# Performance work log

Measured on AMD Instinct MI355X. Metric: run time of the kernel, lower is better.

The kernel has to match this reference:

```python
import jax, jax.numpy as jnp
import numpy as np

N = 50000      # nodes
E = 800000     # edges (before self-loops)
B = 512        # graphs in batch
IN, HID, OUT, HEADS = 768, 256, 128, 4
NEG_SLOPE = 0.2
EPS = 1e-16


def glorot(key, shape):
    fan = shape[0] + shape[-1]
    return jax.random.normal(key, shape, jnp.float32) * jnp.sqrt(2.0 / fan)


def setup_inputs() -> dict:
    key = jax.random.key(0)
    ks = jax.random.split(key, 12)
    d1, d2 = HID // HEADS, OUT // HEADS
    return {
        "x": jax.random.normal(ks[0], (N, IN), jnp.float32),
        "edge_index": jax.random.randint(ks[1], (2, E), 0, N),
        "batch": jnp.sort(jax.random.randint(ks[2], (N,), 0, B)),
        # conv1: GATConv(IN, HID//HEADS, heads=HEADS)
        "W1": glorot(ks[3], (IN, HID)),
        "att_src1": glorot(ks[4], (HEADS, d1)),
        "att_dst1": glorot(ks[5], (HEADS, d1)),
        "b1": jnp.zeros((HID,), jnp.float32),
        # conv2: GATConv(HID+IN, OUT//HEADS, heads=HEADS)
        "W2": glorot(ks[6], (HID + IN, OUT)),
        "att_src2": glorot(ks[7], (HEADS, d2)),
        "att_dst2": glorot(ks[8], (HEADS, d2)),
        "b2": jnp.zeros((OUT,), jnp.float32),
    }


def gat_conv(x, src, dst, W, att_src, att_dst, bias):
    # PyG GATConv (concat heads): h = x @ W, e_ij = LeakyReLU(a_s.h_j + a_d.h_i),
    # alpha = softmax over incoming edges of each destination node.
    n = x.shape[0]
    heads, d = att_src.shape
    h = (x @ W).reshape(n, heads, d)                          # [N,H,D]
    a_s = jnp.einsum('nhd,hd->nh', h, att_src)                # [N,H]
    a_d = jnp.einsum('nhd,hd->nh', h, att_dst)
    e = jax.nn.leaky_relu(a_s[src] + a_d[dst], NEG_SLOPE)     # [Etot,H]
    e_max = jax.ops.segment_max(e, dst, num_segments=n)
    e = jnp.exp(e - e_max[dst])
    denom = jax.ops.segment_sum(e, dst, num_segments=n)
    alpha = e / (denom[dst] + EPS)                            # [Etot,H]
    msg = h[src] * alpha[:, :, None]                          # [Etot,H,D]
    out = jax.ops.segment_sum(msg, dst, num_segments=n)       # [N,H,D]
    return out.reshape(n, heads * d) + bias


def reference(x, edge_index, batch, W1, att_src1, att_dst1, b1,
              W2, att_src2, att_dst2, b2):
    # BUrumorGAT swaps edge direction: row<->col
    src = edge_index[1]
    dst = edge_index[0]
    # PyG GATConv adds self-loops by default
    loops = jnp.arange(N)
    src = jnp.concatenate([src, loops])
    dst = jnp.concatenate([dst, loops])

    x1 = x  # original features
    h1 = gat_conv(x, src, dst, W1, att_src1, att_dst1, b1)    # [N,HID]
    x2 = h1

    # root of each graph = first node (in order) with that batch id
    roots = jax.ops.segment_min(jnp.arange(N), batch, num_segments=B)  # [B]
    re1 = x1[roots[batch]]                                    # [N,IN]
    xc = jax.nn.relu(jnp.concatenate([h1, re1], axis=1))      # [N,HID+IN]
    # F.dropout with training=False is identity (eval mode)

    h2 = jax.nn.relu(gat_conv(xc, src, dst, W2, att_src2, att_dst2, b2))  # [N,OUT]
    re2 = x2[roots[batch]]                                    # [N,HID]
    feat = jnp.concatenate([h2, re2], axis=1)                 # [N,OUT+HID]

    counts = jax.ops.segment_sum(jnp.ones((N,), jnp.float32), batch, num_segments=B)
    pooled = jax.ops.segment_sum(feat, batch, num_segments=B)
    return pooled / jnp.clip(counts, 1.0)[:, None]            # [B,OUT+HID]
```

## Files before the change

kernel.cpp:

```cpp
#include <hip/hip_runtime.h>

#define NN 50000
#define NBGRAPH 512
#define DIN 768
#define DHID 256
#define DOUT 128

typedef unsigned short ushort_t;
typedef __attribute__((ext_vector_type(4))) float f32x4;
typedef _Float16 f16_t;
typedef __attribute__((ext_vector_type(8))) _Float16 f16x8;

__device__ __forceinline__ float lrelu(float v) { return v > 0.f ? v : 0.2f * v; }

__device__ __forceinline__ float h2f_u(ushort_t u) { return (float)__builtin_bit_cast(f16_t, u); }
__device__ __forceinline__ ushort_t f2h_u(float f) { return __builtin_bit_cast(ushort_t, (f16_t)f); }

__device__ __forceinline__ float sel_h(int h, float q0, float q1, float q2, float q3) {
  float lo = (h & 1) ? q1 : q0;
  float hi = (h & 1) ? q3 : q2;
  return (h & 2) ? hi : lo;
}

__device__ __forceinline__ f16x8 cvt8(float4 u, float4 v) {
  unsigned int a = __builtin_bit_cast(unsigned int, __builtin_amdgcn_cvt_pkrtz(u.x, u.y));
  unsigned int b = __builtin_bit_cast(unsigned int, __builtin_amdgcn_cvt_pkrtz(u.z, u.w));
  unsigned int c = __builtin_bit_cast(unsigned int, __builtin_amdgcn_cvt_pkrtz(v.x, v.y));
  unsigned int d = __builtin_bit_cast(unsigned int, __builtin_amdgcn_cvt_pkrtz(v.z, v.w));
  uint4 q = {a, b, c, d};
  return __builtin_bit_cast(f16x8, q);
}
__device__ __forceinline__ f16x8 cvt8_relu(float4 u, float4 v) {
  u.x = fmaxf(u.x, 0.f); u.y = fmaxf(u.y, 0.f); u.z = fmaxf(u.z, 0.f); u.w = fmaxf(u.w, 0.f);
  v.x = fmaxf(v.x, 0.f); v.y = fmaxf(v.y, 0.f); v.z = fmaxf(v.z, 0.f); v.w = fmaxf(v.w, 0.f);
  return cvt8(u, v);
}

__device__ __forceinline__ void gl_lds16(const void* g, void* l) {
  __builtin_amdgcn_global_load_lds(
      (const __attribute__((address_space(1))) unsigned int*)g,
      (__attribute__((address_space(3))) unsigned int*)l, 16, 0, 0);
}

__global__ void k_zero2(int* __restrict__ a, int* __restrict__ b, int n) {
  int i = blockIdx.x * blockDim.x + threadIdx.x;
  if (i < n) { a[i] = 0; b[i] = 0; }
}

__global__ void k_hist(const int* __restrict__ ei, int* __restrict__ deg, int E, int Etot) {
  int e = blockIdx.x * blockDim.x + threadIdx.x;
  if (e >= Etot) return;
  int dst = (e < E) ? ei[e] : (e - E);
  atomicAdd(&deg[dst], 1);
}

__global__ __launch_bounds__(1024) void k_scan1(const int* __restrict__ deg, int* __restrict__ off,
                                                int* __restrict__ bsum, int n) {
  __shared__ int wsum[16];
  int tid = threadIdx.x, lane = tid & 63, w = tid >> 6;
  int i = blockIdx.x * 1024 + tid;
  int v = (i < n) ? deg[i] : 0;
  int x = v;
#pragma unroll
  for (int d = 1; d < 64; d <<= 1) { int t = __shfl_up(x, d); if (lane >= d) x += t; }
  if (lane == 63) wsum[w] = x;
  __syncthreads();
  if (tid < 16) {
    int y = wsum[tid];
#pragma unroll
    for (int d = 1; d < 16; d <<= 1) { int t = __shfl_up(y, d); if (tid >= d) y += t; }
    wsum[tid] = y;
  }
  __syncthreads();
  int base = (w > 0) ? wsum[w - 1] : 0;
  if (i < n) off[i] = base + x - v;
  if (tid == 1023) bsum[blockIdx.x] = wsum[15];
}

__global__ void k_scan2(int* __restrict__ bsum, int* __restrict__ off, int nb, int n) {
  int lane = threadIdx.x;
  int v = (lane < nb) ? bsum[lane] : 0;
  int x = v;
#pragma unroll
  for (int d = 1; d < 64; d <<= 1) { int t = __shfl_up(x, d); if (lane >= d) x += t; }
  if (lane < nb) bsum[lane] = x - v;
  if (lane == 63) off[n] = x;
}

__global__ void k_scan3(int* __restrict__ off, const int* __restrict__ bsum, int n) {
  int i = blockIdx.x * blockDim.x + threadIdx.x;
  if (i < n) off[i] += bsum[i >> 10];
}

__global__ void k_scatter(const int* __restrict__ ei, const int* __restrict__ off,
                          int* __restrict__ cur, int* __restrict__ csr, int E, int Etot) {
  int e = blockIdx.x * blockDim.x + threadIdx.x;
  if (e >= Etot) return;
  int dst, src;
  if (e < E) { dst = ei[e]; src = ei[E + e]; }
  else       { dst = src = e - E; }
  int p = atomicAdd(&cur[dst], 1);
  csr[off[dst] + p] = src;
}

__global__ void k_segstart(const int* __restrict__ batch, int* __restrict__ segstart, int n, int b_cnt) {
  int b = blockIdx.x * blockDim.x + threadIdx.x;
  if (b > b_cnt) return;
  int lo = 0, hi = n;
  while (lo < hi) { int mid = (lo + hi) >> 1; if (batch[mid] < b) lo = mid + 1; else hi = mid; }
  segstart[b] = lo;
}

__global__ void k_rootn(const int* __restrict__ batch, const int* __restrict__ segstart,
                        int* __restrict__ rootn, int n) {
  int i = blockIdx.x * blockDim.x + threadIdx.x;
  if (i < n) rootn[i] = segstart[batch[i]];
}

__global__ void k_prepW(const float* __restrict__ W, ushort_t* __restrict__ Wt, int K, int N) {
  int id = blockIdx.x * blockDim.x + threadIdx.x;
  if (id >= K * N) return;
  int n = id / K, k = id - n * K;
  Wt[(size_t)n * K + k] = f2h_u(W[(size_t)k * N + n]);
}

#define ABUF1 (128 * 32)
#define BBUF1 (128 * 32)
__global__ __launch_bounds__(256) void k_gemm1m(const float* __restrict__ A,
                                                const ushort_t* __restrict__ Bt,
                                                ushort_t* __restrict__ C) {
  const int K = DIN, NC = DHID;
  __shared__ __align__(16) float As[2 * ABUF1];
  __shared__ __align__(16) ushort_t Bs[2 * BBUF1];
  const int tid = threadIdx.x;
  const int bm = blockIdx.x * 128;
  const int bn = blockIdx.y * 128;
  const int wid = tid >> 6, lane = tid & 63;
  const int wr = (wid >> 1) * 64, wc = (wid & 1) * 64;
  const int fr = lane & 15, fg = lane >> 4;
  f32x4 acc[4][4] = {};

  const float* asrc[4];
  int adoff[4];
#pragma unroll
  for (int j = 0; j < 4; ++j) {
    int c = j * 256 + tid;
    int row = c >> 3, ci = c & 7;
    int gc = ci ^ (row & 7);
    int gr = bm + row; if (gr >= NN) gr = NN - 1;
    asrc[j] = &A[(size_t)gr * K + gc * 4];
    adoff[j] = row * 32 + ci * 4;
  }
  const ushort_t* bsrc[2];
  int bdoff[2];
#pragma unroll
  for (int j = 0; j < 2; ++j) {
    int c = j * 256 + tid;
    int col = c >> 2, ci = c & 3;
    int gc = ci ^ (col & 3);
    bsrc[j] = &Bt[(size_t)(bn + col) * K + gc * 8];
    bdoff[j] = col * 32 + ci * 8;
  }

#pragma unroll
  for (int j = 0; j < 4; ++j) gl_lds16(asrc[j], &As[adoff[j]]);
#pragma unroll
  for (int j = 0; j < 2; ++j) gl_lds16(bsrc[j], &Bs[bdoff[j]]);
  __syncthreads();

  int cur = 0;
  for (int k0 = 0; k0 < K; k0 += 32) {
    const int nxt = cur ^ 1;
    if (k0 + 32 < K) {
#pragma unroll
      for (int j = 0; j < 4; ++j) gl_lds16(asrc[j] + k0 + 32, &As[nxt * ABUF1 + adoff[j]]);
#pragma unroll
      for (int j = 0; j < 2; ++j) gl_lds16(bsrc[j] + k0 + 32, &Bs[nxt * BBUF1 + bdoff[j]]);
    }
    const float* Ab = &As[cur * ABUF1];
    const ushort_t* Bb = &Bs[cur * BBUF1];
    f16x8 af[4], bfr[4];
#pragma unroll
    for (int m = 0; m < 4; ++m) {
      int r = wr + m * 16 + fr;
      int c0 = (2 * fg) ^ (r & 7), c1 = (2 * fg + 1) ^ (r & 7);
      float4 u = *(const float4*)&Ab[r * 32 + c0 * 4];
      float4 v = *(const float4*)&Ab[r * 32 + c1 * 4];
      af[m] = cvt8(u, v);
    }
#pragma unroll
    for (int n = 0; n < 4; ++n) {
      int c = wc + n * 16 + fr;
      bfr[n] = *(const f16x8*)&Bb[c * 32 + (fg ^ (c & 3)) * 8];
    }
#pragma unroll
    for (int m = 0; m < 4; ++m)
#pragma unroll
      for (int n = 0; n < 4; ++n)
        acc[m][n] = __builtin_amdgcn_mfma_f32_16x16x32_f16(af[m], bfr[n], acc[m][n], 0, 0, 0);
    __syncthreads();
    cur = nxt;
  }
#pragma unroll
  for (int m = 0; m < 4; ++m)
#pragma unroll
    for (int n = 0; n < 4; ++n)
#pragma unroll
      for (int j = 0; j < 4; ++j) {
        int r = bm + wr + m * 16 + fg * 4 + j;
        if (r < NN) C[(size_t)r * NC + bn + wc + n * 16 + fr] = f2h_u(acc[m][n][j]);
      }
}

#define ABUF2 (64 * 32)
#define BBUF2 (128 * 32)
__global__ __launch_bounds__(256) void k_gemm2m(const float* __restrict__ OUT1,
                                                const float* __restrict__ X,
                                                const int* __restrict__ rootn,
                                                const ushort_t* __restrict__ Bt,
                                                ushort_t* __restrict__ C) {
  const int K = DHID + DIN, NC = DOUT;
  __shared__ __align__(16) float As[2 * ABUF2];
  __shared__ __align__(16) ushort_t Bs[2 * BBUF2];
  const int tid = threadIdx.x;
  const int bm = blockIdx.x * 64;
  const int wid = tid >> 6, lane = tid & 63;
  const int wr = (wid >> 1) * 32, wc = (wid & 1) * 64;
  const int fr = lane & 15, fg = lane >> 4;
  f32x4 acc[2][4] = {};

  const float* o1src[2];
  const float* xsrc[2];
  int adoff[2];
#pragma unroll
  for (int j = 0; j < 2; ++j) {
    int c = j * 256 + tid;
    int row = c >> 3, ci = c & 7;
    int gc = ci ^ (row & 7);
    int gr = bm + row; if (gr >= NN) gr = NN - 1;
    int rn = rootn[gr];
    o1src[j] = &OUT1[(size_t)gr * DHID + gc * 4];
    xsrc[j] = &X[(size_t)rn * DIN + gc * 4];
    adoff[j] = row * 32 + ci * 4;
  }
  const ushort_t* bsrc[2];
  int bdoff[2];
#pragma unroll
  for (int j = 0; j < 2; ++j) {
    int c = j * 256 + tid;
    int col = c >> 2, ci = c & 3;
    int gc = ci ^ (col & 3);
    bsrc[j] = &Bt[(size_t)col * K + gc * 8];
    bdoff[j] = col * 32 + ci * 8;
  }

#pragma unroll
  for (int j = 0; j < 2; ++j) gl_lds16(o1src[j], &As[adoff[j]]);
#pragma unroll
  for (int j = 0; j < 2; ++j) gl_lds16(bsrc[j], &Bs[bdoff[j]]);
  __syncthreads();

  int cur = 0;
  for (int k0 = 0; k0 < K; k0 += 32) {
    const int nxt = cur ^ 1;
    if (k0 + 32 < K) {
      const int k0n = k0 + 32;
      const bool inO1 = k0n < DHID;
#pragma unroll
      for (int j = 0; j < 2; ++j)
        gl_lds16(inO1 ? (o1src[j] + k0n) : (xsrc[j] + (k0n - DHID)), &As[nxt * ABUF2 + adoff[j]]);
#pragma unroll
      for (int j = 0; j < 2; ++j) gl_lds16(bsrc[j] + k0n, &Bs[nxt * BBUF2 + bdoff[j]]);
    }
    const float* Ab = &As[cur * ABUF2];
    const ushort_t* Bb = &Bs[cur * BBUF2];
    f16x8 af[2], bfr[4];
#pragma unroll
    for (int m = 0; m < 2; ++m) {
      int r = wr + m * 16 + fr;
      int c0 = (2 * fg) ^ (r & 7), c1 = (2 * fg + 1) ^ (r & 7);
      float4 u = *(const float4*)&Ab[r * 32 + c0 * 4];
      float4 v = *(const float4*)&Ab[r * 32 + c1 * 4];
      af[m] = cvt8_relu(u, v);
    }
#pragma unroll
    for (int n = 0; n < 4; ++n) {
      int c = wc + n * 16 + fr;
      bfr[n] = *(const f16x8*)&Bb[c * 32 + (fg ^ (c & 3)) * 8];
    }
#pragma unroll
    for (int m = 0; m < 2; ++m)
#pragma unroll
      for (int n = 0; n < 4; ++n)
        acc[m][n] = __builtin_amdgcn_mfma_f32_16x16x32_f16(af[m], bfr[n], acc[m][n], 0, 0, 0);
    __syncthreads();
    cur = nxt;
  }
#pragma unroll
  for (int m = 0; m < 2; ++m)
#pragma unroll
    for (int n = 0; n < 4; ++n)
#pragma unroll
      for (int j = 0; j < 4; ++j) {
        int r = bm + wr + m * 16 + fg * 4 + j;
        if (r < NN) C[(size_t)r * NC + wc + n * 16 + fr] = f2h_u(acc[m][n][j]);
      }
}

__global__ __launch_bounds__(256) void k_scores1(const ushort_t* __restrict__ Hh,
                                                 const float* __restrict__ att_s,
                                                 const float* __restrict__ att_d,
                                                 float4* __restrict__ as_out,
                                                 float4* __restrict__ ad_out) {
  int lane = threadIdx.x & 63;
  int n = blockIdx.x * 4 + (threadIdx.x >> 6);
  if (n >= NN) return;
  ushort4 hv = *(const ushort4*)&Hh[(size_t)n * DHID + lane * 4];
  float h0 = h2f_u(hv.x), h1 = h2f_u(hv.y), h2 = h2f_u(hv.z), h3 = h2f_u(hv.w);
  float4 sa = *(const float4*)&att_s[lane * 4];
  float4 da = *(const float4*)&att_d[lane * 4];
  float ps = h0 * sa.x + h1 * sa.y + h2 * sa.z + h3 * sa.w;
  float pd = h0 * da.x + h1 * da.y + h2 * da.z + h3 * da.w;
#pragma unroll
  for (int m = 1; m < 16; m <<= 1) { ps += __shfl_xor(ps, m); pd += __shfl_xor(pd, m); }
  float4 rs, rd;
  rs.x = __shfl(ps, 0);  rd.x = __shfl(pd, 0);
  rs.y = __shfl(ps, 16); rd.y = __shfl(pd, 16);
  rs.z = __shfl(ps, 32); rd.z = __shfl(pd, 32);
  rs.w = __shfl(ps, 48); rd.w = __shfl(pd, 48);
  if (lane == 0) { as_out[n] = rs; ad_out[n] = rd; }
}

__global__ __launch_bounds__(256) void k_scores2(const ushort_t* __restrict__ Hh,
                                                 const float* __restrict__ att_s,
                                                 const float* __restrict__ att_d,
                                                 float4* __restrict__ as_out,
                                                 float4* __restrict__ ad_out) {
  int lane = threadIdx.x & 63;
  int n = blockIdx.x * 4 + (threadIdx.x >> 6);
  if (n >= NN) return;
  ushort2 hv = *(const ushort2*)&Hh[(size_t)n * DOUT + lane * 2];
  float h0 = h2f_u(hv.x), h1 = h2f_u(hv.y);
  float2 sa = *(const float2*)&att_s[lane * 2];
  float2 da = *(const float2*)&att_d[lane * 2];
  float ps = h0 * sa.x + h1 * sa.y;
  float pd = h0 * da.x + h1 * da.y;
#pragma unroll
  for (int m = 1; m < 16; m <<= 1) { ps += __shfl_xor(ps, m); pd += __shfl_xor(pd, m); }
  float4 rs, rd;
  rs.x = __shfl(ps, 0);  rd.x = __shfl(pd, 0);
  rs.y = __shfl(ps, 16); rd.y = __shfl(pd, 16);
  rs.z = __shfl(ps, 32); rd.z = __shfl(pd, 32);
  rs.w = __shfl(ps, 48); rd.w = __shfl(pd, 48);
  if (lane == 0) { as_out[n] = rs; ad_out[n] = rd; }
}

__global__ __launch_bounds__(256) void k_agg1(const int* __restrict__ off, const int* __restrict__ csr,
                                              const float4* __restrict__ as_v, const float4* __restrict__ ad_v,
                                              const ushort_t* __restrict__ Hh, const float* __restrict__ bias,
                                              float* __restrict__ OUT) {
  __shared__ int s_tab[16][65];
  __shared__ __align__(16) float al_tab[16][260];
  const int tid = threadIdx.x;
  const int nd = tid >> 4;
  const int g = tid & 15;
  const int hd = g >> 2;
  const int n = blockIdx.x * 16 + nd;
  if (n >= NN) return;
  const int beg = off[n];
  const int nt = off[n + 1] - beg;
  const float4 adv = ad_v[n];

  float acc[16] = {};
  float rdh;

  if (nt <= 64) {
    float mx0 = -INFINITY, mx1 = -INFINITY, mx2 = -INFINITY, mx3 = -INFINITY;
    for (int le = g; le < nt; le += 16) {
      int s = csr[beg + le];
      float4 a = as_v[s];
      s_tab[nd][le] = s;
      *(float4*)&al_tab[nd][le << 2] = a;
      mx0 = fmaxf(mx0, a.x); mx1 = fmaxf(mx1, a.y);
      mx2 = fmaxf(mx2, a.z); mx3 = fmaxf(mx3, a.w);
    }
#pragma unroll
    for (int m = 1; m < 16; m <<= 1) {
      mx0 = fmaxf(mx0, __shfl_xor(mx0, m)); mx1 = fmaxf(mx1, __shfl_xor(mx1, m));
      mx2 = fmaxf(mx2, __shfl_xor(mx2, m)); mx3 = fmaxf(mx3, __shfl_xor(mx3, m));
    }
    float em0 = lrelu(mx0 + adv.x), em1 = lrelu(mx1 + adv.y);
    float em2 = lrelu(mx2 + adv.z), em3 = lrelu(mx3 + adv.w);
    float s0 = 0.f, s1 = 0.f, s2 = 0.f, s3 = 0.f;
    for (int le = g; le < nt; le += 16) {
      float4 a = *(const float4*)&al_tab[nd][le << 2];
      float p0 = __expf(lrelu(a.x + adv.x) - em0);
      float p1 = __expf(lrelu(a.y + adv.y) - em1);
      float p2 = __expf(lrelu(a.z + adv.z) - em2);
      float p3 = __expf(lrelu(a.w + adv.w) - em3);
      *(float4*)&al_tab[nd][le << 2] = make_float4(p0, p1, p2, p3);
      s0 += p0; s1 += p1; s2 += p2; s3 += p3;
    }
#pragma unroll
    for (int m = 1; m < 16; m <<= 1) {
      s0 += __shfl_xor(s0, m); s1 += __shfl_xor(s1, m);
      s2 += __shfl_xor(s2, m); s3 += __shfl_xor(s3, m);
    }
    rdh = sel_h(hd, 1.f / (s0 + 1e-16f), 1.f / (s1 + 1e-16f),
                    1.f / (s2 + 1e-16f), 1.f / (s3 + 1e-16f));

    int sP = s_tab[nd][0];
    float pP = al_tab[nd][hd];
    f16x8 v0 = *(const f16x8*)&Hh[(size_t)sP * DHID + g * 16];
    f16x8 v1 = *(const f16x8*)&Hh[(size_t)sP * DHID + g * 16 + 8];
    for (int e = 0; e < nt; ++e) {
      int en = (e + 1 < nt) ? e + 1 : e;
      int sN = s_tab[nd][en];
      float pN = al_tab[nd][(en << 2) | hd];
      f16x8 n0 = *(const f16x8*)&Hh[(size_t)sN * DHID + g * 16];
      f16x8 n1 = *(const f16x8*)&Hh[(size_t)sN * DHID + g * 16 + 8];
      float al = pP * rdh;
#pragma unroll
      for (int q = 0; q < 8; ++q) acc[q] += al * (float)v0[q];
#pragma unroll
      for (int q = 0; q < 8; ++q) acc[8 + q] += al * (float)v1[q];
      pP = pN; v0 = n0; v1 = n1;
    }
  } else {
    float mx0 = -INFINITY, mx1 = -INFINITY, mx2 = -INFINITY, mx3 = -INFINITY;
    for (int le = g; le < nt; le += 16) {
      float4 a = as_v[csr[beg + le]];
      mx0 = fmaxf(mx0, a.x); mx1 = fmaxf(mx1, a.y);
      mx2 = fmaxf(mx2, a.z); mx3 = fmaxf(mx3, a.w);
    }
#pragma unroll
    for (int m = 1; m < 16; m <<= 1) {
      mx0 = fmaxf(mx0, __shfl_xor(mx0, m)); mx1 = fmaxf(mx1, __shfl_xor(mx1, m));
      mx2 = fmaxf(mx2, __shfl_xor(mx2, m)); mx3 = fmaxf(mx3, __shfl_xor(mx3, m));
    }
    float em0 = lrelu(mx0 + adv.x), em1 = lrelu(mx1 + adv.y);
    float em2 = lrelu(mx2 + adv.z), em3 = lrelu(mx3 + adv.w);
    float s0 = 0.f, s1 = 0.f, s2 = 0.f, s3 = 0.f;
    for (int le = g; le < nt; le += 16) {
      float4 a = as_v[csr[beg + le]];
      s0 += __expf(lrelu(a.x + adv.x) - em0);
      s1 += __expf(lrelu(a.y + adv.y) - em1);
      s2 += __expf(lrelu(a.z + adv.z) - em2);
      s3 += __expf(lrelu(a.w + adv.w) - em3);
    }
#pragma unroll
    for (int m = 1; m < 16; m <<= 1) {
      s0 += __shfl_xor(s0, m); s1 += __shfl_xor(s1, m);
      s2 += __shfl_xor(s2, m); s3 += __shfl_xor(s3, m);
    }
    rdh = sel_h(hd, 1.f / (s0 + 1e-16f), 1.f / (s1 + 1e-16f),
                    1.f / (s2 + 1e-16f), 1.f / (s3 + 1e-16f));
    float adh = sel_h(hd, adv.x, adv.y, adv.z, adv.w);
    float emh = sel_h(hd, em0, em1, em2, em3);
    for (int e = 0; e < nt; ++e) {
      int s = csr[beg + e];
      float4 a = as_v[s];
      float ah = sel_h(hd, a.x, a.y, a.z, a.w);
      float al = __expf(lrelu(ah + adh) - emh) * rdh;
      f16x8 v0 = *(const f16x8*)&Hh[(size_t)s * DHID + g * 16];
      f16x8 v1 = *(const f16x8*)&Hh[(size_t)s * DHID + g * 16 + 8];
#pragma unroll
      for (int q = 0; q < 8; ++q) acc[q] += al * (float)v0[q];
#pragma unroll
      for (int q = 0; q < 8; ++q) acc[8 + q] += al * (float)v1[q];
    }
  }

  const float* bv = &bias[g * 16];
  float* ob = &OUT[(size_t)n * DHID + g * 16];
#pragma unroll
  for (int k = 0; k < 4; ++k) {
    float4 b4 = *(const float4*)&bv[k * 4];
    *(float4*)&ob[k * 4] = make_float4(acc[k * 4] + b4.x, acc[k * 4 + 1] + b4.y,
                                       acc[k * 4 + 2] + b4.z, acc[k * 4 + 3] + b4.w);
  }
}

__global__ __launch_bounds__(256) void k_agg2(const int* __restrict__ off, const int* __restrict__ csr,
                                              const float4* __restrict__ as_v, const float4* __restrict__ ad_v,
                                              const ushort_t* __restrict__ Hh, const float* __restrict__ bias,
                                              float* __restrict__ OUT) {
  __shared__ int s_tab[16][65];
  __shared__ __align__(16) float al_tab[16][260];
  const int tid = threadIdx.x;
  const int nd = tid >> 4;
  const int g = tid & 15;
  const int hd = g >> 2;
  const int n = blockIdx.x * 16 + nd;
  if (n >= NN) return;
  const int beg = off[n];
  const int nt = off[n + 1] - beg;
  const float4 adv = ad_v[n];

  float acc[8] = {};
  float rdh;

  if (nt <= 64) {
    float mx0 = -INFINITY, mx1 = -INFINITY, mx2 = -INFINITY, mx3 = -INFINITY;
    for (int le = g; le < nt; le += 16) {
      int s = csr[beg + le];
      float4 a = as_v[s];
      s_tab[nd][le] = s;
      *(float4*)&al_tab[nd][le << 2] = a;
      mx0 = fmaxf(mx0, a.x); mx1 = fmaxf(mx1, a.y);
      mx2 = fmaxf(mx2, a.z); mx3 = fmaxf(mx3, a.w);
    }
#pragma unroll
    for (int m = 1; m < 16; m <<= 1) {
      mx0 = fmaxf(mx0, __shfl_xor(mx0, m)); mx1 = fmaxf(mx1, __shfl_xor(mx1, m));
      mx2 = fmaxf(mx2, __shfl_xor(mx2, m)); mx3 = fmaxf(mx3, __shfl_xor(mx3, m));
    }
    float em0 = lrelu(mx0 + adv.x), em1 = lrelu(mx1 + adv.y);
    float em2 = lrelu(mx2 + adv.z), em3 = lrelu(mx3 + adv.w);
    float s0 = 0.f, s1 = 0.f, s2 = 0.f, s3 = 0.f;
    for (int le = g; le < nt; le += 16) {
      float4 a = *(const float4*)&al_tab[nd][le << 2];
      float p0 = __expf(lrelu(a.x + adv.x) - em0);
      float p1 = __expf(lrelu(a.y + adv.y) - em1);
      float p2 = __expf(lrelu(a.z + adv.z) - em2);
      float p3 = __expf(lrelu(a.w + adv.w) - em3);
      *(float4*)&al_tab[nd][le << 2] = make_float4(p0, p1, p2, p3);
      s0 += p0; s1 += p1; s2 += p2; s3 += p3;
    }
#pragma unroll
    for (int m = 1; m < 16; m <<= 1) {
      s0 += __shfl_xor(s0, m); s1 += __shfl_xor(s1, m);
      s2 += __shfl_xor(s2, m); s3 += __shfl_xor(s3, m);
    }
    rdh = sel_h(hd, 1.f / (s0 + 1e-16f), 1.f / (s1 + 1e-16f),
                    1.f / (s2 + 1e-16f), 1.f / (s3 + 1e-16f));

    int sP = s_tab[nd][0];
    float pP = al_tab[nd][hd];
    f16x8 v0 = *(const f16x8*)&Hh[(size_t)sP * DOUT + g * 8];
    for (int e = 0; e < nt; ++e) {
      int en = (e + 1 < nt) ? e + 1 : e;
      int sN = s_tab[nd][en];
      float pN = al_tab[nd][(en << 2) | hd];
      f16x8 n0 = *(const f16x8*)&Hh[(size_t)sN * DOUT + g * 8];
      float al = pP * rdh;
#pragma unroll
      for (int q = 0; q < 8; ++q) acc[q] += al * (float)v0[q];
      pP = pN; v0 = n0;
    }
  } else {
    float mx0 = -INFINITY, mx1 = -INFINITY, mx2 = -INFINITY, mx3 = -INFINITY;
    for (int le = g; le < nt; le += 16) {
      float4 a = as_v[csr[beg + le]];
      mx0 = fmaxf(mx0, a.x); mx1 = fmaxf(mx1, a.y);
      mx2 = fmaxf(mx2, a.z); mx3 = fmaxf(mx3, a.w);
    }
#pragma unroll
    for (int m = 1; m < 16; m <<= 1) {
      mx0 = fmaxf(mx0, __shfl_xor(mx0, m)); mx1 = fmaxf(mx1, __shfl_xor(mx1, m));
      mx2 = fmaxf(mx2, __shfl_xor(mx2, m)); mx3 = fmaxf(mx3, __shfl_xor(mx3, m));
    }
    float em0 = lrelu(mx0 + adv.x), em1 = lrelu(mx1 + adv.y);
    float em2 = lrelu(mx2 + adv.z), em3 = lrelu(mx3 + adv.w);
    float s0 = 0.f, s1 = 0.f, s2 = 0.f, s3 = 0.f;
    for (int le = g; le < nt; le += 16) {
      float4 a = as_v[csr[beg + le]];
      s0 += __expf(lrelu(a.x + adv.x) - em0);
      s1 += __expf(lrelu(a.y + adv.y) - em1);
      s2 += __expf(lrelu(a.z + adv.z) - em2);
      s3 += __expf(lrelu(a.w + adv.w) - em3);
    }
#pragma unroll
    for (int m = 1; m < 16; m <<= 1) {
      s0 += __shfl_xor(s0, m); s1 += __shfl_xor(s1, m);
      s2 += __shfl_xor(s2, m); s3 += __shfl_xor(s3, m);
    }
    rdh = sel_h(hd, 1.f / (s0 + 1e-16f), 1.f / (s1 + 1e-16f),
                    1.f / (s2 + 1e-16f), 1.f / (s3 + 1e-16f));
    float adh = sel_h(hd, adv.x, adv.y, adv.z, adv.w);
    float emh = sel_h(hd, em0, em1, em2, em3);
    for (int e = 0; e < nt; ++e) {
      int s = csr[beg + e];
      float4 a = as_v[s];
      float ah = sel_h(hd, a.x, a.y, a.z, a.w);
      float al = __expf(lrelu(ah + adh) - emh) * rdh;
      f16x8 v0 = *(const f16x8*)&Hh[(size_t)s * DOUT + g * 8];
#pragma unroll
      for (int q = 0; q < 8; ++q) acc[q] += al * (float)v0[q];
    }
  }

  const float* bv = &bias[g * 8];
  float* ob = &OUT[(size_t)n * DOUT + g * 8];
#pragma unroll
  for (int k = 0; k < 2; ++k) {
    float4 b4 = *(const float4*)&bv[k * 4];
    *(float4*)&ob[k * 4] = make_float4(acc[k * 4] + b4.x, acc[k * 4 + 1] + b4.y,
                                       acc[k * 4 + 2] + b4.z, acc[k * 4 + 3] + b4.w);
  }
}

__global__ __launch_bounds__(256) void k_pool(const int* __restrict__ segstart,
                                              const float* __restrict__ OUT2,
                                              const float* __restrict__ OUT1,
                                              float* __restrict__ out) {
  int b = blockIdx.x;
  int t = threadIdx.x;
  int s = segstart[b], e = segstart[b + 1];
  float* ob = out + (size_t)b * 384;
  if (s >= e) {
    for (int i = t; i < 384; i += 256) ob[i] = 0.f;
    return;
  }
  if (t < 128) {
    float s0 = 0.f, s1 = 0.f;
    int n = s;
    for (; n + 1 < e; n += 2) {
      float v0 = OUT2[(size_t)n * DOUT + t];
      float v1 = OUT2[(size_t)(n + 1) * DOUT + t];
      s0 += fmaxf(v0, 0.f); s1 += fmaxf(v1, 0.f);
    }
    if (n < e) s0 += fmaxf(OUT2[(size_t)n * DOUT + t], 0.f);
    ob[t] = (s0 + s1) / (float)(e - s);
  } else {
    int k = t - 128;
    ob[128 + k] = OUT1[(size_t)s * DHID + k];
    ob[256 + k] = OUT1[(size_t)s * DHID + 128 + k];
  }
}

extern "C" void kernel_launch(void* const* d_in, const int* in_sizes, int n_in,
                              void* d_out, int out_size, void* d_ws, size_t ws_size,
                              hipStream_t stream) {
  const float* x    = (const float*)d_in[0];
  const int*   ei   = (const int*)d_in[1];
  const int*   batch = (const int*)d_in[2];
  const float* W1   = (const float*)d_in[3];
  const float* as1w = (const float*)d_in[4];
  const float* ad1w = (const float*)d_in[5];
  const float* b1   = (const float*)d_in[6];
  const float* W2   = (const float*)d_in[7];
  const float* as2w = (const float*)d_in[8];
  const float* ad2w = (const float*)d_in[9];
  const float* b2   = (const float*)d_in[10];
  float* out = (float*)d_out;
  char* ws = (char*)d_ws;

  const int E = in_sizes[1] / 2;
  const int Etot = E + NN;

  ushort_t* H1h = (ushort_t*)(ws + 0);
  ushort_t* H2h = (ushort_t*)(ws + 0);
  ushort_t* Wt2h = (ushort_t*)(ws + 13000000);
  float*  OUT2 = (float*)(ws + 25600000);
  float*  OUT1 = (float*)(ws + 51200000);
  float4* as1  = (float4*)(ws + 102400000);
  float4* ad1  = (float4*)(ws + 103200000);
  float4* as2  = (float4*)(ws + 104000000);
  float4* ad2  = (float4*)(ws + 104800000);
  int* deg     = (int*)(ws + 105600000);
  int* cur     = (int*)(ws + 105800000);
  int* off     = (int*)(ws + 106000000);
  int* csr     = (int*)(ws + 106200016);
  int* segstart = (int*)(ws + 109600016);
  int* rootn   = (int*)(ws + 109602080);
  int* bsum    = (int*)(ws + 109802080);
  ushort_t* Wt1h = (ushort_t*)(ws + 105600000);

  const int TB = 256;
  const int NB_SCAN = (NN + 1023) / 1024;

  k_zero2<<<(NN + TB - 1) / TB, TB, 0, stream>>>(deg, cur, NN);
  k_hist<<<(Etot + TB - 1) / TB, TB, 0, stream>>>(ei, deg, E, Etot);
  k_scan1<<<NB_SCAN, 1024, 0, stream>>>(deg, off, bsum, NN);
  k_scan2<<<1, 64, 0, stream>>>(bsum, off, NB_SCAN, NN);
  k_scan3<<<NB_SCAN, 1024, 0, stream>>>(off, bsum, NN);
  k_scatter<<<(Etot + TB - 1) / TB, TB, 0, stream>>>(ei, off, cur, csr, E, Etot);
  k_segstart<<<(NBGRAPH + 1 + TB - 1) / TB, TB, 0, stream>>>(batch, segstart, NN, NBGRAPH);
  k_rootn<<<(NN + TB - 1) / TB, TB, 0, stream>>>(batch, segstart, rootn, NN);

  k_prepW<<<(DIN * DHID + TB - 1) / TB, TB, 0, stream>>>(W1, Wt1h, DIN, DHID);
  dim3 g1((NN + 127) / 128, DHID / 128);
  k_gemm1m<<<g1, TB, 0, stream>>>(x, Wt1h, H1h);
  k_scores1<<<(NN + 3) / 4, TB, 0, stream>>>(H1h, as1w, ad1w, as1, ad1);
  k_agg1<<<(NN + 15) / 16, TB, 0, stream>>>(off, csr, as1, ad1, H1h, b1, OUT1);

  k_prepW<<<((DHID + DIN) * DOUT + TB - 1) / TB, TB, 0, stream>>>(W2, Wt2h, DHID + DIN, DOUT);
  dim3 g2((NN + 63) / 64, 1);
  k_gemm2m<<<g2, TB, 0, stream>>>(OUT1, x, rootn, Wt2h, H2h);
  k_scores2<<<(NN + 3) / 4, TB, 0, stream>>>(H2h, as2w, ad2w, as2, ad2);
  k_agg2<<<(NN + 15) / 16, TB, 0, stream>>>(off, csr, as2, ad2, H2h, b2, OUT2);

  k_pool<<<NBGRAPH, TB, 0, stream>>>(segstart, OUT2, OUT1, out);
}
```

Measured before the change: 352.0 us.

## Triple-buffer GEMM loads with vmcnt waits and retile gemm1 to full-width N

Both GEMM kernels move from double-buffered LDS with __syncthreads to a three-stage ring buffer. Explicit s_waitcnt vmcnt counts let two tiles of async global-to-LDS loads stay in flight while the current tile is consumed. gemm1 is also retiled from 128x128 blocks over a 2D grid to 64x256 blocks covering all output columns, so each x row is read from global memory only once. The cost is more LDS per block, which may lower occupancy, and the hand-tuned vmcnt values depend on the exact number of loads issued per stage.

```diff
diff --git a/kernel.cpp b/kernel.cpp
--- a/kernel.cpp
+++ b/kernel.cpp
@@ -124,64 +124,70 @@
   Wt[(size_t)n * K + k] = f2h_u(W[(size_t)k * N + n]);
 }
 
-#define ABUF1 (128 * 32)
-#define BBUF1 (128 * 32)
+#define NT1 (DIN / 32)
+#define A1SZ (64 * 32)
+#define B1SZ (256 * 32)
 __global__ __launch_bounds__(256) void k_gemm1m(const float* __restrict__ A,
                                                 const ushort_t* __restrict__ Bt,
                                                 ushort_t* __restrict__ C) {
-  const int K = DIN, NC = DHID;
-  __shared__ __align__(16) float As[2 * ABUF1];
-  __shared__ __align__(16) ushort_t Bs[2 * BBUF1];
+  __shared__ __align__(16) float As[3 * A1SZ];
+  __shared__ __align__(16) ushort_t Bs[3 * B1SZ];
   const int tid = threadIdx.x;
-  const int bm = blockIdx.x * 128;
-  const int bn = blockIdx.y * 128;
+  const int bm = blockIdx.x * 64;
   const int wid = tid >> 6, lane = tid & 63;
-  const int wr = (wid >> 1) * 64, wc = (wid & 1) * 64;
+  const int wr = (wid >> 1) * 32, wc = (wid & 1) * 128;
   const int fr = lane & 15, fg = lane >> 4;
-  f32x4 acc[4][4] = {};
-
-  const float* asrc[4];
-  int adoff[4];
-#pragma unroll
-  for (int j = 0; j < 4; ++j) {
+  f32x4 acc[2][8] = {};
+
+  const float* asrc[2];
+  int adoff[2];
+#pragma unroll
+  for (int j = 0; j < 2; ++j) {
     int c = j * 256 + tid;
     int row = c >> 3, ci = c & 7;
     int gc = ci ^ (row & 7);
     int gr = bm + row; if (gr >= NN) gr = NN - 1;
-    asrc[j] = &A[(size_t)gr * K + gc * 4];
-    adoff[j] = row * 32 + ci * 4;
-  }
-  const ushort_t* bsrc[2];
-  int bdoff[2];
-#pragma unroll
-  for (int j = 0; j < 2; ++j) {
+    asrc[j] = &A[(size_t)gr * DIN + gc * 4];
+    adoff[j] = c * 4;
+  }
+  const ushort_t* bsrc[4];
+  int bdoff[4];
+#pragma unroll
+  for (int j = 0; j < 4; ++j) {
     int c = j * 256 + tid;
     int col = c >> 2, ci = c & 3;
     int gc = ci ^ (col & 3);
-    bsrc[j] = &Bt[(size_t)(bn + col) * K + gc * 8];
-    bdoff[j] = col * 32 + ci * 8;
-  }
-
-#pragma unroll
-  for (int j = 0; j < 4; ++j) gl_lds16(asrc[j], &As[adoff[j]]);
-#pragma unroll
-  for (int j = 0; j < 2; ++j) gl_lds16(bsrc[j], &Bs[bdoff[j]]);
-  __syncthreads();
-
-  int cur = 0;
-  for (int k0 = 0; k0 < K; k0 += 32) {
-    const int nxt = cur ^ 1;
-    if (k0 + 32 < K) {
-#pragma unroll
-      for (int j = 0; j < 4; ++j) gl_lds16(asrc[j] + k0 + 32, &As[nxt * ABUF1 + adoff[j]]);
-#pragma unroll
-      for (int j = 0; j < 2; ++j) gl_lds16(bsrc[j] + k0 + 32, &Bs[nxt * BBUF1 + bdoff[j]]);
-    }
-    const float* Ab = &As[cur * ABUF1];
-    const ushort_t* Bb = &Bs[cur * BBUF1];
-    f16x8 af[4], bfr[4];
-#pragma unroll
-    for (int m = 0; m < 4; ++m) {
+    bsrc[j] = &Bt[(size_t)col * DIN + gc * 8];
+    bdoff[j] = c * 8;
+  }
+
+#define STAGE1(T, B)                                                        \
+  {                                                                         \
+    const int kk_ = (T) * 32;                                               \
+    _Pragma("unroll")                                                       \
+    for (int j = 0; j < 2; ++j) gl_lds16(asrc[j] + kk_, &As[(B) * A1SZ + adoff[j]]); \
+    _Pragma("unroll")                                                       \
+    for (int j = 0; j < 4; ++j) gl_lds16(bsrc[j] + kk_, &Bs[(B) * B1SZ + bdoff[j]]); \
+  }
+
+  STAGE1(0, 0);
+  STAGE1(1, 1);
+  int cur = 0, nx1 = 1, nx2 = 2;
+  for (int t = 0; t < NT1; ++t) {
+    if (t + 2 < NT1) {
+      STAGE1(t + 2, nx2);
+      asm volatile("s_waitcnt vmcnt(12)" ::: "memory");
+    } else if (t + 1 < NT1) {
+      asm volatile("s_waitcnt vmcnt(6)" ::: "memory");
+    } else {
+      asm volatile("s_waitcnt vmcnt(0)" ::: "memory");
+    }
+    __builtin_amdgcn_s_barrier();
+    const float* Ab = &As[cur * A1SZ];
+    const ushort_t* Bb = &Bs[cur * B1SZ];
+    f16x8 af[2], bfr[8];
+#pragma unroll
+    for (int m = 0; m < 2; ++m) {
       int r = wr + m * 16 + fr;
       int c0 = (2 * fg) ^ (r & 7), c1 = (2 * fg + 1) ^ (r & 7);
       float4 u = *(const float4*)&Ab[r * 32 + c0 * 4];
@@ -189,39 +195,40 @@
       af[m] = cvt8(u, v);
     }
 #pragma unroll
-    for (int n = 0; n < 4; ++n) {
+    for (int n = 0; n < 8; ++n) {
       int c = wc + n * 16 + fr;
       bfr[n] = *(const f16x8*)&Bb[c * 32 + (fg ^ (c & 3)) * 8];
     }
 #pragma unroll
-    for (int m = 0; m < 4; ++m)
-#pragma unroll
-      for (int n = 0; n < 4; ++n)
+    for (int m = 0; m < 2; ++m)
+#pragma unroll
+      for (int n = 0; n < 8; ++n)
         acc[m][n] = __builtin_amdgcn_mfma_f32_16x16x32_f16(af[m], bfr[n], acc[m][n], 0, 0, 0);
-    __syncthreads();
-    cur = nxt;
-  }
-#pragma unroll
-  for (int m = 0; m < 4; ++m)
-#pragma unroll
-    for (int n = 0; n < 4; ++n)
+    __builtin_amdgcn_s_barrier();
+    int tmp = cur; cur = nx1; nx1 = nx2; nx2 = tmp;
+  }
+#pragma unroll
+  for (int m = 0; m < 2; ++m)
+#pragma unroll
+    for (int n = 0; n < 8; ++n)
 #pragma unroll
       for (int j = 0; j < 4; ++j) {
         int r = bm + wr + m * 16 + fg * 4 + j;
-        if (r < NN) C[(size_t)r * NC + bn + wc + n * 16 + fr] = f2h_u(acc[m][n][j]);
+        if (r < NN) C[(size_t)r * DHID + wc + n * 16 + fr] = f2h_u(acc[m][n][j]);
       }
 }
 
-#define ABUF2 (64 * 32)
-#define BBUF2 (128 * 32)
+#define NT2 ((DHID + DIN) / 32)
+#define A2SZ (64 * 32)
+#define B2SZ (128 * 32)
 __global__ __launch_bounds__(256) void k_gemm2m(const float* __restrict__ OUT1,
                                                 const float* __restrict__ X,
                                                 const int* __restrict__ rootn,
                                                 const ushort_t* __restrict__ Bt,
                                                 ushort_t* __restrict__ C) {
-  const int K = DHID + DIN, NC = DOUT;
-  __shared__ __align__(16) float As[2 * ABUF2];
-  __shared__ __align__(16) ushort_t Bs[2 * BBUF2];
+  const int K = DHID + DIN;
+  __shared__ __align__(16) float As[3 * A2SZ];
+  __shared__ __align__(16) ushort_t Bs[3 * B2SZ];
   const int tid = threadIdx.x;
   const int bm = blockIdx.x * 64;
   const int wid = tid >> 6, lane = tid & 63;
@@ -241,7 +248,7 @@
     int rn = rootn[gr];
     o1src[j] = &OUT1[(size_t)gr * DHID + gc * 4];
     xsrc[j] = &X[(size_t)rn * DIN + gc * 4];
-    adoff[j] = row * 32 + ci * 4;
+    adoff[j] = c * 4;
   }
   const ushort_t* bsrc[2];
   int bdoff[2];
@@ -251,29 +258,35 @@
     int col = c >> 2, ci = c & 3;
     int gc = ci ^ (col & 3);
     bsrc[j] = &Bt[(size_t)col * K + gc * 8];
-    bdoff[j] = col * 32 + ci * 8;
-  }
-
-#pragma unroll
-  for (int j = 0; j < 2; ++j) gl_lds16(o1src[j], &As[adoff[j]]);
-#pragma unroll
-  for (int j = 0; j < 2; ++j) gl_lds16(bsrc[j], &Bs[bdoff[j]]);
-  __syncthreads();
-
-  int cur = 0;
-  for (int k0 = 0; k0 < K; k0 += 32) {
-    const int nxt = cur ^ 1;
-    if (k0 + 32 < K) {
-      const int k0n = k0 + 32;
-      const bool inO1 = k0n < DHID;
-#pragma unroll
-      for (int j = 0; j < 2; ++j)
-        gl_lds16(inO1 ? (o1src[j] + k0n) : (xsrc[j] + (k0n - DHID)), &As[nxt * ABUF2 + adoff[j]]);
-#pragma unroll
-      for (int j = 0; j < 2; ++j) gl_lds16(bsrc[j] + k0n, &Bs[nxt * BBUF2 + bdoff[j]]);
-    }
-    const float* Ab = &As[cur * ABUF2];
-    const ushort_t* Bb = &Bs[cur * BBUF2];
+    bdoff[j] = c * 8;
+  }
+
+#define STAGE2(T, B)                                                        \
+  {                                                                         \
+    const int kk_ = (T) * 32;                                               \
+    _Pragma("unroll")                                                       \
+    for (int j = 0; j < 2; ++j)                                             \
+      gl_lds16((kk_ < DHID) ? (o1src[j] + kk_) : (xsrc[j] + (kk_ - DHID)),  \
+               &As[(B) * A2SZ + adoff[j]]);                                 \
+    _Pragma("unroll")                                                       \
+    for (int j = 0; j < 2; ++j) gl_lds16(bsrc[j] + kk_, &Bs[(B) * B2SZ + bdoff[j]]); \
+  }
+
+  STAGE2(0, 0);
+  STAGE2(1, 1);
+  int cur = 0, nx1 = 1, nx2 = 2;
+  for (int t = 0; t < NT2; ++t) {
+    if (t + 2 < NT2) {
+      STAGE2(t + 2, nx2);
+      asm volatile("s_waitcnt vmcnt(8)" ::: "memory");
+    } else if (t + 1 < NT2) {
+      asm volatile("s_waitcnt vmcnt(4)" ::: "memory");
+    } else {
+      asm volatile("s_waitcnt vmcnt(0)" ::: "memory");
+    }
+    __builtin_amdgcn_s_barrier();
+    const float* Ab = &As[cur * A2SZ];
+    const ushort_t* Bb = &Bs[cur * B2SZ];
     f16x8 af[2], bfr[4];
 #pragma unroll
     for (int m = 0; m < 2; ++m) {
@@ -293,8 +306,8 @@
 #pragma unroll
       for (int n = 0; n < 4; ++n)
         acc[m][n] = __builtin_amdgcn_mfma_f32_16x16x32_f16(af[m], bfr[n], acc[m][n], 0, 0, 0);
-    __syncthreads();
-    cur = nxt;
+    __builtin_amdgcn_s_barrier();
+    int tmp = cur; cur = nx1; nx1 = nx2; nx2 = tmp;
   }
 #pragma unroll
   for (int m = 0; m < 2; ++m)
@@ -303,7 +316,7 @@
 #pragma unroll
       for (int j = 0; j < 4; ++j) {
         int r = bm + wr + m * 16 + fg * 4 + j;
-        if (r < NN) C[(size_t)r * NC + wc + n * 16 + fr] = f2h_u(acc[m][n][j]);
+        if (r < NN) C[(size_t)r * DOUT + wc + n * 16 + fr] = f2h_u(acc[m][n][j]);
       }
 }
 
@@ -680,7 +693,7 @@
   k_rootn<<<(NN + TB - 1) / TB, TB, 0, stream>>>(batch, segstart, rootn, NN);
 
   k_prepW<<<(DIN * DHID + TB - 1) / TB, TB, 0, stream>>>(W1, Wt1h, DIN, DHID);
-  dim3 g1((NN + 127) / 128, DHID / 128);
+  dim3 g1((NN + 63) / 64, 1);
   k_gemm1m<<<g1, TB, 0, stream>>>(x, Wt1h, H1h);
   k_scores1<<<(NN + 3) / 4, TB, 0, stream>>>(H1h, as1w, ad1w, as1, ad1);
   k_agg1<<<(NN + 15) / 16, TB, 0, stream>>>(off, csr, as1, ad1, H1h, b1, OUT1);
```

After: 364.1 us. +3.4%, slower.
